# Performance work log

Measured on AMD Instinct MI355X. Metric: run time of the kernel, lower is better.

## Reference

```python
import jax, jax.numpy as jnp
import numpy as np

N = 50000       # nodes
E = 800000      # edges (before self-loops)
IN = 64         # in_channels
OUT = 64        # out_channels


def setup_inputs() -> dict:
    key = jax.random.key(0)
    ks = jax.random.split(key, 6)
    X = jax.random.normal(ks[0], (N, IN), jnp.float32)
    H = jax.random.normal(ks[1], (N, OUT), jnp.float32)
    edge_index = jax.random.randint(ks[2], (2, E), 0, N, dtype=jnp.int64)
    edge_weight = jax.random.uniform(ks[3], (E,), jnp.float32)
    fan_in = IN + OUT
    W1 = jax.random.normal(ks[4], (fan_in, 2 * OUT), jnp.float32) / np.sqrt(fan_in).astype(np.float32)
    b1 = jnp.ones((2 * OUT,), jnp.float32)   # TGCN sets graph_conv1.bias to ones
    W2 = jax.random.normal(ks[5], (fan_in, OUT), jnp.float32) / np.sqrt(fan_in).astype(np.float32)
    b2 = jnp.zeros((OUT,), jnp.float32)      # default GCNConv bias init
    return {"X": X, "H": H, "edge_index": edge_index, "edge_weight": edge_weight,
            "W1": W1, "b1": b1, "W2": W2, "b2": b2}


def _gcn_conv(x, W, b, src, dst, w, n):
    """PyG GCNConv: linear transform, add self-loops (fill=1, improved=False),
    symmetric deg^-1/2 normalization, scatter-add aggregation at dst, + bias."""
    x = x @ W                                   # [N, out]
    loop = jnp.arange(n, dtype=src.dtype)
    s = jnp.concatenate([src, loop])            # [E+N]
    d = jnp.concatenate([dst, loop])
    ww = jnp.concatenate([w, jnp.ones((n,), x.dtype)])
    deg = jax.ops.segment_sum(ww, d, num_segments=n)
    dinv = jnp.where(deg > 0, jax.lax.rsqrt(jnp.maximum(deg, 1e-12)), 0.0)
    norm = dinv[s] * ww * dinv[d]               # [E+N]
    msg = x[s] * norm[:, None]                  # gather + scale
    out = jax.ops.segment_sum(msg, d, num_segments=n)  # scatter-add at dst
    return out + b


def reference(X, H, edge_index, edge_weight, W1, b1, W2, b2):
    src, dst = edge_index[0], edge_index[1]
    n = X.shape[0]
    ru = jax.nn.sigmoid(_gcn_conv(jnp.concatenate([X, H], axis=1), W1, b1, src, dst, edge_weight, n))
    r, u = ru[:, :OUT], ru[:, OUT:]             # chunk into reset/update gates
    c = jnp.tanh(_gcn_conv(jnp.concatenate([X, H * r], axis=1), W2, b2, src, dst, edge_weight, n))
    return u * H + (1.0 - u) * c                # new hidden state [N, OUT]
```

## Files before the change

### kernel.cpp

```cpp
#include <hip/hip_runtime.h>
#include <hip/hip_bf16.h>
#include <hip/hip_fp16.h>

#define NN 50000
#define NE 800000
#define NBIN ((NN + 255) / 256)
#define PB ((NE + 1023) / 1024)
#define GB ((NN + 63) / 64)
#define MAXB 4864

__device__ __forceinline__ unsigned int f2bf(float x) {
    unsigned int u = __float_as_uint(x);
    return (u + 0x7FFFu + ((u >> 16) & 1u)) >> 16;
}
__device__ __forceinline__ float bf2f(unsigned int b) {
    return __uint_as_float(b << 16);
}

template <int OUTC, int NKC, int SRC, int OMODE>
__device__ __forceinline__ void gemm_core(
    const float* __restrict__ X, const float* __restrict__ Hm,
    const unsigned int* __restrict__ RUb, const float* __restrict__ W,
    const float* __restrict__ addF, const float* __restrict__ dinvp,
    uint2* __restrict__ outB, float* __restrict__ outF,
    int bid, float4* wS4, float4* inS4)
{
    constexpr int CG = OUTC / 4;
    constexpr int RSTEP = 256 / CG;
    constexpr int RPT = 64 / RSTEP;
    const int tid = threadIdx.x;
    const int cg = tid % CG;
    const int rsub = tid / CG;
    const int row0 = bid * 64;

    float4 acc[RPT];
    #pragma unroll
    for (int r = 0; r < RPT; ++r) acc[r] = {0.f, 0.f, 0.f, 0.f};

    for (int kc = 0; kc < NKC; ++kc) {
        const float4* Wg = reinterpret_cast<const float4*>(W + kc * 16 * OUTC);
        #pragma unroll
        for (int i = tid; i < 16 * CG; i += 256) wS4[i] = Wg[i];
        {
            int rr = tid >> 2, j = tid & 3;
            int row = row0 + rr;
            float4 v = {0.f, 0.f, 0.f, 0.f};
            if (row < NN) {
                int f4 = kc * 4 + j;
                if (SRC == 0) {
                    v = (f4 < 16) ? reinterpret_cast<const float4*>(X)[row * 16 + f4]
                                  : reinterpret_cast<const float4*>(Hm)[row * 16 + f4 - 16];
                } else if (SRC == 1) {
                    v = reinterpret_cast<const float4*>(X)[row * 16 + f4];
                } else {
                    v = reinterpret_cast<const float4*>(Hm)[row * 16 + f4];
                    unsigned int r0 = RUb[row * 64 + 2 * f4];
                    unsigned int r1 = RUb[row * 64 + 2 * f4 + 1];
                    v.x *= bf2f(r0 & 0xFFFFu); v.y *= bf2f(r0 >> 16);
                    v.z *= bf2f(r1 & 0xFFFFu); v.w *= bf2f(r1 >> 16);
                }
            }
            inS4[rr * 4 + j] = v;
        }
        __syncthreads();

        #pragma unroll
        for (int k8 = 0; k8 < 2; ++k8) {
            float4 wr[8];
            #pragma unroll
            for (int j = 0; j < 8; ++j) wr[j] = wS4[(k8 * 8 + j) * CG + cg];
            #pragma unroll
            for (int r = 0; r < RPT; ++r) {
                const int rr = rsub + r * RSTEP;
                float4 a0 = inS4[rr * 4 + k8 * 2];
                float4 a1 = inS4[rr * 4 + k8 * 2 + 1];
                acc[r].x += a0.x * wr[0].x; acc[r].y += a0.x * wr[0].y;
                acc[r].z += a0.x * wr[0].z; acc[r].w += a0.x * wr[0].w;
                acc[r].x += a0.y * wr[1].x; acc[r].y += a0.y * wr[1].y;
                acc[r].z += a0.y * wr[1].z; acc[r].w += a0.y * wr[1].w;
                acc[r].x += a0.z * wr[2].x; acc[r].y += a0.z * wr[2].y;
                acc[r].z += a0.z * wr[2].z; acc[r].w += a0.z * wr[2].w;
                acc[r].x += a0.w * wr[3].x; acc[r].y += a0.w * wr[3].y;
                acc[r].z += a0.w * wr[3].z; acc[r].w += a0.w * wr[3].w;
                acc[r].x += a1.x * wr[4].x; acc[r].y += a1.x * wr[4].y;
                acc[r].z += a1.x * wr[4].z; acc[r].w += a1.x * wr[4].w;
                acc[r].x += a1.y * wr[5].x; acc[r].y += a1.y * wr[5].y;
                acc[r].z += a1.y * wr[5].z; acc[r].w += a1.y * wr[5].w;
                acc[r].x += a1.z * wr[6].x; acc[r].y += a1.z * wr[6].y;
                acc[r].z += a1.z * wr[6].z; acc[r].w += a1.z * wr[6].w;
                acc[r].x += a1.w * wr[7].x; acc[r].y += a1.w * wr[7].y;
                acc[r].z += a1.w * wr[7].z; acc[r].w += a1.w * wr[7].w;
            }
        }
        __syncthreads();
    }

    #pragma unroll
    for (int r = 0; r < RPT; ++r) {
        int row = row0 + rsub + r * RSTEP;
        if (row < NN) {
            if (OMODE == 1) {
                reinterpret_cast<float4*>(outF)[(size_t)row * CG + cg] = acc[r];
            } else {
                float4 a = acc[r];
                if (OMODE == 2) {
                    float4 ad = reinterpret_cast<const float4*>(addF)[(size_t)row * CG + cg];
                    float dv = dinvp[row];
                    a.x = (a.x + ad.x) * dv; a.y = (a.y + ad.y) * dv;
                    a.z = (a.z + ad.z) * dv; a.w = (a.w + ad.w) * dv;
                }
                uint2 o;
                o.x = f2bf(a.x) | (f2bf(a.y) << 16);
                o.y = f2bf(a.z) | (f2bf(a.w) << 16);
                outB[(size_t)row * CG + cg] = o;
            }
        }
    }
}

__launch_bounds__(256)
__global__ void k_build(const float* __restrict__ X, const float* __restrict__ Hm,
                        const float* __restrict__ W1, const float* __restrict__ W2,
                        uint2* __restrict__ Z1b, float* __restrict__ Z2p,
                        const int* __restrict__ dst, int* __restrict__ HT) {
    __shared__ float4 wS4[512];
    __shared__ float4 inS4[256];
    const int bid = blockIdx.x;
    const int tid = threadIdx.x;
    if (bid < PB) {
        int* hist = reinterpret_cast<int*>(wS4);
        for (int i = tid; i < NBIN; i += 256) hist[i] = 0;
        __syncthreads();
        const int base = bid * 1024 + tid;
        #pragma unroll
        for (int k = 0; k < 4; ++k) {
            int e = base + k * 256;
            if (e < NE) atomicAdd(&hist[dst[e] >> 8], 1);
        }
        __syncthreads();
        for (int i = tid; i < NBIN; i += 256) HT[i * PB + bid] = hist[i];
        return;
    }
    if (bid < PB + GB) {
        gemm_core<128, 8, 0, 0>(X, Hm, nullptr, W1, nullptr, nullptr, Z1b, nullptr,
                                bid - PB, wS4, inS4);
        return;
    }
    gemm_core<64, 4, 1, 1>(X, Hm, nullptr, W2, nullptr, nullptr, nullptr, Z2p,
                           bid - PB - GB, wS4, inS4);
}

__launch_bounds__(256)
__global__ void k_scanA1(const int* __restrict__ HT, int* __restrict__ within,
                         int* __restrict__ binTot) {
    __shared__ int lds[PB];
    __shared__ int sc[256];
    __shared__ int carryS;
    const int b = blockIdx.x, tid = threadIdx.x;
    if (tid == 0) carryS = 0;
    for (int i = tid; i < PB; i += 256) lds[i] = HT[b * PB + i];
    __syncthreads();
    for (int c0 = 0; c0 < PB; c0 += 256) {
        int i = c0 + tid;
        int v = (i < PB) ? lds[i] : 0;
        sc[tid] = v;
        __syncthreads();
        #pragma unroll
        for (int off = 1; off < 256; off <<= 1) {
            int t = (tid >= off) ? sc[tid - off] : 0;
            __syncthreads();
            sc[tid] += t;
            __syncthreads();
        }
        int carry = carryS;
        if (i < PB) lds[i] = carry + sc[tid] - v;
        __syncthreads();
        if (tid == 255) carryS = carry + sc[255];
        __syncthreads();
    }
    for (int i = tid; i < PB; i += 256) within[b * PB + i] = lds[i];
    if (tid == 0) binTot[b] = carryS;
}

__launch_bounds__(256)
__global__ void k_scanA2(const int* __restrict__ binTot, int* __restrict__ binStart) {
    __shared__ int sc[256];
    const int tid = threadIdx.x;
    int v = (tid < NBIN) ? binTot[tid] : 0;
    sc[tid] = v;
    __syncthreads();
    #pragma unroll
    for (int off = 1; off < 256; off <<= 1) {
        int t = (tid >= off) ? sc[tid - off] : 0;
        __syncthreads();
        sc[tid] += t;
        __syncthreads();
    }
    if (tid < NBIN) binStart[tid] = sc[tid] - v;
    if (tid == 0) binStart[NBIN] = NE;
}

__launch_bounds__(256)
__global__ void k_scatterA(const int* __restrict__ src, const int* __restrict__ dst,
                           const float* __restrict__ w, const int* __restrict__ binStart,
                           const int* __restrict__ within, uint2* __restrict__ rec) {
    __shared__ int cur[NBIN];
    const int blk = blockIdx.x, tid = threadIdx.x;
    for (int b = tid; b < NBIN; b += 256) cur[b] = binStart[b] + within[b * PB + blk];
    __syncthreads();
    const int base = blk * 1024 + tid;
    #pragma unroll
    for (int k = 0; k < 4; ++k) {
        int e = base + k * 256;
        if (e < NE) {
            int d = dst[e];
            int pos = atomicAdd(&cur[d >> 8], 1);
            unsigned int hn = __half_as_ushort(__float2half(w[e]));
            uint2 r;
            r.x = (unsigned int)src[e] | (hn << 16);
            r.y = (unsigned int)d;
            rec[pos] = r;
        }
    }
}

__launch_bounds__(256)
__global__ void k_phase2(const uint2* __restrict__ rec, const int* __restrict__ binStart,
                         unsigned int* __restrict__ snP, int* __restrict__ start,
                         float* __restrict__ dinv, uint2* __restrict__ Z1b) {
    __shared__ unsigned int rSn[MAXB];
    __shared__ unsigned char rLo[MAXB];
    __shared__ unsigned int outSn[MAXB];
    __shared__ int cnt[256];
    __shared__ int sc[256];
    __shared__ int lstart[256];
    __shared__ int cur[256];
    __shared__ float dls[256];
    const int b = blockIdx.x, tid = threadIdx.x;
    const int e0 = binStart[b];
    int nE = binStart[b + 1] - e0;
    if (nE > MAXB) nE = MAXB;

    cnt[tid] = 0;
    __syncthreads();
    for (int i = tid; i < nE; i += 256) {
        uint2 r = rec[e0 + i];
        rSn[i] = r.x;
        int lo = r.y & 255;
        rLo[i] = (unsigned char)lo;
        atomicAdd(&cnt[lo], 1);
    }
    __syncthreads();
    sc[tid] = cnt[tid];
    __syncthreads();
    #pragma unroll
    for (int off = 1; off < 256; off <<= 1) {
        int t = (tid >= off) ? sc[tid - off] : 0;
        __syncthreads();
        sc[tid] += t;
        __syncthreads();
    }
    lstart[tid] = sc[tid] - cnt[tid];
    cur[tid] = sc[tid] - cnt[tid];
    __syncthreads();
    const int node = b * 256 + tid;
    if (node <= NN) start[node] = e0 + lstart[tid];
    for (int i = tid; i < nE; i += 256) {
        int p = atomicAdd(&cur[rLo[i]], 1);
        outSn[p] = rSn[i];
    }
    __syncthreads();
    for (int i = tid; i < nE; i += 256) snP[e0 + i] = outSn[i];
    {
        int s0 = lstart[tid], c = cnt[tid];
        float sum = 0.f;
        for (int i = s0; i < s0 + c; ++i)
            sum += __half2float(__ushort_as_half((unsigned short)(outSn[i] >> 16)));
        float dv = rsqrtf(1.0f + sum);
        dls[tid] = dv;
        if (node < NN) dinv[node] = dv;
    }
    __syncthreads();
    const int nLoc = (NN - b * 256 < 256) ? (NN - b * 256) : 256;
    for (int i = tid; i < nLoc * 32; i += 256) {
        int l = i >> 5, j = i & 31;
        size_t g = (size_t)(b * 256 + l) * 32 + j;
        uint2 z = Z1b[g];
        float dv = dls[l];
        float z0 = bf2f(z.x & 0xFFFFu) * dv, z1 = bf2f(z.x >> 16) * dv;
        float z2 = bf2f(z.y & 0xFFFFu) * dv, z3 = bf2f(z.y >> 16) * dv;
        uint2 o;
        o.x = f2bf(z0) | (f2bf(z1) << 16);
        o.y = f2bf(z2) | (f2bf(z3) << 16);
        Z1b[g] = o;
    }
}

__launch_bounds__(256)
__global__ void k_gemm2b(const float* __restrict__ X, const float* __restrict__ Hm,
                         const unsigned int* __restrict__ RUb, const float* __restrict__ W2,
                         const float* __restrict__ Z2p, const float* __restrict__ dinv,
                         uint2* __restrict__ Z2b) {
    __shared__ float4 wS4[256];
    __shared__ float4 inS4[256];
    gemm_core<64, 4, 2, 2>(X, Hm, RUb, W2 + 64 * 64, Z2p, dinv, Z2b, nullptr,
                           blockIdx.x, wS4, inS4);
}

template <int OUTC, int MODE>
__launch_bounds__(256)
__global__ void k_gather(const int* __restrict__ start, const unsigned int* __restrict__ snP,
                         const uint2* __restrict__ Zb, const float* __restrict__ dinv,
                         const float* __restrict__ bias, const uint2* __restrict__ RUb2,
                         uint2* __restrict__ outB, const float* __restrict__ Hm,
                         float* __restrict__ out) {
    constexpr int GRP = OUTC / 4;
    constexpr int NPB = 256 / GRP;
    const int node = blockIdx.x * NPB + threadIdx.x / GRP;
    const int l = threadIdx.x % GRP;
    if (node >= NN) return;

    const int e0 = start[node], e1 = start[node + 1];

    uint2 zs = Zb[(size_t)node * GRP + l];
    float4 acc;
    acc.x = bf2f(zs.x & 0xFFFFu);
    acc.y = bf2f(zs.x >> 16);
    acc.z = bf2f(zs.y & 0xFFFFu);
    acc.w = bf2f(zs.y >> 16);

    #define EFMA(Z, NM) \
        acc.x += bf2f((Z).x & 0xFFFFu) * (NM); \
        acc.y += bf2f((Z).x >> 16) * (NM);     \
        acc.z += bf2f((Z).y & 0xFFFFu) * (NM); \
        acc.w += bf2f((Z).y >> 16) * (NM);

    int e = e0;
    for (; e + 8 <= e1; e += 8) {
        unsigned sn0 = snP[e],     sn1 = snP[e + 1], sn2 = snP[e + 2], sn3 = snP[e + 3];
        unsigned sn4 = snP[e + 4], sn5 = snP[e + 5], sn6 = snP[e + 6], sn7 = snP[e + 7];
        uint2 z0 = Zb[(size_t)(sn0 & 0xFFFFu) * GRP + l];
        uint2 z1 = Zb[(size_t)(sn1 & 0xFFFFu) * GRP + l];
        uint2 z2 = Zb[(size_t)(sn2 & 0xFFFFu) * GRP + l];
        uint2 z3 = Zb[(size_t)(sn3 & 0xFFFFu) * GRP + l];
        uint2 z4 = Zb[(size_t)(sn4 & 0xFFFFu) * GRP + l];
        uint2 z5 = Zb[(size_t)(sn5 & 0xFFFFu) * GRP + l];
        uint2 z6 = Zb[(size_t)(sn6 & 0xFFFFu) * GRP + l];
        uint2 z7 = Zb[(size_t)(sn7 & 0xFFFFu) * GRP + l];
        float n0 = __half2float(__ushort_as_half((unsigned short)(sn0 >> 16)));
        float n1 = __half2float(__ushort_as_half((unsigned short)(sn1 >> 16)));
        float n2 = __half2float(__ushort_as_half((unsigned short)(sn2 >> 16)));
        float n3 = __half2float(__ushort_as_half((unsigned short)(sn3 >> 16)));
        float n4 = __half2float(__ushort_as_half((unsigned short)(sn4 >> 16)));
        float n5 = __half2float(__ushort_as_half((unsigned short)(sn5 >> 16)));
        float n6 = __half2float(__ushort_as_half((unsigned short)(sn6 >> 16)));
        float n7 = __half2float(__ushort_as_half((unsigned short)(sn7 >> 16)));
        EFMA(z0, n0) EFMA(z1, n1) EFMA(z2, n2) EFMA(z3, n3)
        EFMA(z4, n4) EFMA(z5, n5) EFMA(z6, n6) EFMA(z7, n7)
    }
    if (e + 4 <= e1) {
        unsigned sn0 = snP[e], sn1 = snP[e + 1], sn2 = snP[e + 2], sn3 = snP[e + 3];
        uint2 z0 = Zb[(size_t)(sn0 & 0xFFFFu) * GRP + l];
        uint2 z1 = Zb[(size_t)(sn1 & 0xFFFFu) * GRP + l];
        uint2 z2 = Zb[(size_t)(sn2 & 0xFFFFu) * GRP + l];
        uint2 z3 = Zb[(size_t)(sn3 & 0xFFFFu) * GRP + l];
        float n0 = __half2float(__ushort_as_half((unsigned short)(sn0 >> 16)));
        float n1 = __half2float(__ushort_as_half((unsigned short)(sn1 >> 16)));
        float n2 = __half2float(__ushort_as_half((unsigned short)(sn2 >> 16)));
        float n3 = __half2float(__ushort_as_half((unsigned short)(sn3 >> 16)));
        EFMA(z0, n0) EFMA(z1, n1) EFMA(z2, n2) EFMA(z3, n3)
        e += 4;
    }
    for (; e < e1; ++e) {
        unsigned sn = snP[e];
        float nm = __half2float(__ushort_as_half((unsigned short)(sn >> 16)));
        uint2 z = Zb[(size_t)(sn & 0xFFFFu) * GRP + l];
        EFMA(z, nm)
    }
    #undef EFMA

    const float dv = dinv[node];
    const int c = l * 4;
    float4 bb = *reinterpret_cast<const float4*>(bias + c);
    acc.x = acc.x * dv + bb.x; acc.y = acc.y * dv + bb.y;
    acc.z = acc.z * dv + bb.z; acc.w = acc.w * dv + bb.w;

    if (MODE == 0) {
        float4 o;
        o.x = 1.f / (1.f + expf(-acc.x));
        o.y = 1.f / (1.f + expf(-acc.y));
        o.z = 1.f / (1.f + expf(-acc.z));
        o.w = 1.f / (1.f + expf(-acc.w));
        uint2 pk;
        pk.x = f2bf(o.x) | (f2bf(o.y) << 16);
        pk.y = f2bf(o.z) | (f2bf(o.w) << 16);
        outB[(size_t)node * 32 + l] = pk;
    } else {
        uint2 uu = RUb2[(size_t)node * 32 + 16 + l];
        float u0 = bf2f(uu.x & 0xFFFFu), u1 = bf2f(uu.x >> 16);
        float u2 = bf2f(uu.y & 0xFFFFu), u3 = bf2f(uu.y >> 16);
        float4 h4 = *reinterpret_cast<const float4*>(Hm + (size_t)node * 64 + c);
        float4 o;
        o.x = u0 * h4.x + (1.f - u0) * tanhf(acc.x);
        o.y = u1 * h4.y + (1.f - u1) * tanhf(acc.y);
        o.z = u2 * h4.z + (1.f - u2) * tanhf(acc.z);
        o.w = u3 * h4.w + (1.f - u3) * tanhf(acc.w);
        *reinterpret_cast<float4*>(out + (size_t)node * 64 + c) = o;
    }
}

extern "C" void kernel_launch(void* const* d_in, const int* in_sizes, int n_in,
                              void* d_out, int out_size, void* d_ws, size_t ws_size,
                              hipStream_t stream) {
    const float* X  = (const float*)d_in[0];
    const float* Hm = (const float*)d_in[1];
    const int*   ei = (const int*)d_in[2];
    const float* w  = (const float*)d_in[3];
    const float* W1 = (const float*)d_in[4];
    const float* b1 = (const float*)d_in[5];
    const float* W2 = (const float*)d_in[6];
    const float* b2 = (const float*)d_in[7];
    float* out = (float*)d_out;

    const int* src = ei;
    const int* dst = ei + NE;

    char* p = (char*)d_ws;
    uint2* rec   = (uint2*)p;  p += sizeof(uint2) * NE;
    uint2* Z1b   = (uint2*)p;  p += sizeof(uint2) * NN * 32;
    uint2* Z2b   = (uint2*)p;  p += sizeof(uint2) * NN * 16;
    uint2* RUb2  = (uint2*)p;  p += sizeof(uint2) * NN * 32;
    float* Z2p   = (float*)p;  p += sizeof(float) * NN * 64;
    float* dinv  = (float*)p;  p += sizeof(float) * NN;
    int*   start = (int*)p;    p += sizeof(int) * (NN + 1);
    int*   binTot   = (int*)p; p += sizeof(int) * NBIN;
    int*   binStart = (int*)p; p += sizeof(int) * (NBIN + 1);
    int*   HT       = (int*)p; p += sizeof(int) * NBIN * PB;
    int*   within   = (int*)p; p += sizeof(int) * NBIN * PB;
    unsigned int* snP = (unsigned int*)p; p += sizeof(unsigned int) * NE;

    k_build<<<PB + 2 * GB, 256, 0, stream>>>(X, Hm, W1, W2, Z1b, Z2p, dst, HT);

    k_scanA1<<<NBIN, 256, 0, stream>>>(HT, within, binTot);
    k_scanA2<<<1, 256, 0, stream>>>(binTot, binStart);
    k_scatterA<<<PB, 256, 0, stream>>>(src, dst, w, binStart, within, rec);
    k_phase2<<<NBIN, 256, 0, stream>>>(rec, binStart, snP, start, dinv, Z1b);

    k_gather<128, 0><<<(NN * 32 + 255) / 256, 256, 0, stream>>>(
        start, snP, Z1b, dinv, b1, nullptr, RUb2, nullptr, nullptr);

    k_gemm2b<<<GB, 256, 0, stream>>>(X, Hm, (const unsigned int*)RUb2, W2, Z2p, dinv, Z2b);
    k_gather<64, 1><<<(NN * 16 + 255) / 256, 256, 0, stream>>>(
        start, snP, Z2b, dinv, b2, RUb2, nullptr, Hm, out);
}
```

Measured before the change: 140.6 us.

## Replace FP32 FMA GEMMs with bf16 MFMA using prepacked weight fragments

Adds a small kernel that converts W1 and W2 to bf16 and lays them out in MFMA fragment order. The three dense GEMMs now stage bf16 input tiles in LDS and run 16x16x32 bf16 MFMA instructions instead of scalar FP32 FMAs. This removes the scalar-FMA compute cost of the GEMM stages but adds an extra kernel launch. Inputs are also rounded to bf16 before multiplying, which lowers precision, and the epilogue now writes scalar 16-bit stores instead of packed vector stores.

```diff
diff --git a/kernel.cpp b/kernel.cpp
--- a/kernel.cpp
+++ b/kernel.cpp
@@ -9,6 +9,9 @@
 #define GB ((NN + 63) / 64)
 #define MAXB 4864
 
+typedef __attribute__((ext_vector_type(8))) short bf16x8;
+typedef __attribute__((ext_vector_type(4))) float f32x4;
+
 __device__ __forceinline__ unsigned int f2bf(float x) {
     unsigned int u = __float_as_uint(x);
     return (u + 0x7FFFu + ((u >> 16) & 1u)) >> 16;
@@ -17,118 +20,134 @@
     return __uint_as_float(b << 16);
 }
 
-template <int OUTC, int NKC, int SRC, int OMODE>
-__device__ __forceinline__ void gemm_core(
+__global__ void k_wprep(const float* __restrict__ W1, const float* __restrict__ W2,
+                        unsigned short* __restrict__ Wf1,
+                        unsigned short* __restrict__ Wf2t,
+                        unsigned short* __restrict__ Wf2b) {
+    int i = blockIdx.x * 256 + threadIdx.x;
+    if (i < 16384) {
+        int j = i & 7, l = (i >> 3) & 63, n = (i >> 9) & 7, kc = i >> 12;
+        int k = kc * 32 + ((l >> 4) << 3) + j;
+        int col = (n << 4) + (l & 15);
+        Wf1[i] = (unsigned short)f2bf(W1[k * 128 + col]);
+    }
+    if (i < 4096) {
+        int j = i & 7, l = (i >> 3) & 63, n = (i >> 9) & 3, kc = i >> 11;
+        int k = kc * 32 + ((l >> 4) << 3) + j;
+        int col = (n << 4) + (l & 15);
+        Wf2t[i] = (unsigned short)f2bf(W2[k * 64 + col]);
+        Wf2b[i] = (unsigned short)f2bf(W2[(k + 64) * 64 + col]);
+    }
+}
+
+template <int OUTC, int KC, int SRC, int OMODE>
+__device__ __forceinline__ void mgemm_core(
     const float* __restrict__ X, const float* __restrict__ Hm,
-    const unsigned int* __restrict__ RUb, const float* __restrict__ W,
-    const float* __restrict__ addF, const float* __restrict__ dinvp,
-    uint2* __restrict__ outB, float* __restrict__ outF,
-    int bid, float4* wS4, float4* inS4)
+    const unsigned int* __restrict__ RUb, const unsigned short* __restrict__ Wf,
+    const float* __restrict__ Z2p, const float* __restrict__ dinv,
+    unsigned short* __restrict__ outH, float* __restrict__ outF,
+    int bid, unsigned short* aS, unsigned short* wS)
 {
-    constexpr int CG = OUTC / 4;
-    constexpr int RSTEP = 256 / CG;
-    constexpr int RPT = 64 / RSTEP;
+    constexpr int NT = OUTC / 16;
     const int tid = threadIdx.x;
-    const int cg = tid % CG;
-    const int rsub = tid / CG;
     const int row0 = bid * 64;
 
-    float4 acc[RPT];
-    #pragma unroll
-    for (int r = 0; r < RPT; ++r) acc[r] = {0.f, 0.f, 0.f, 0.f};
-
-    for (int kc = 0; kc < NKC; ++kc) {
-        const float4* Wg = reinterpret_cast<const float4*>(W + kc * 16 * OUTC);
-        #pragma unroll
-        for (int i = tid; i < 16 * CG; i += 256) wS4[i] = Wg[i];
-        {
-            int rr = tid >> 2, j = tid & 3;
-            int row = row0 + rr;
-            float4 v = {0.f, 0.f, 0.f, 0.f};
-            if (row < NN) {
-                int f4 = kc * 4 + j;
-                if (SRC == 0) {
-                    v = (f4 < 16) ? reinterpret_cast<const float4*>(X)[row * 16 + f4]
-                                  : reinterpret_cast<const float4*>(Hm)[row * 16 + f4 - 16];
-                } else if (SRC == 1) {
-                    v = reinterpret_cast<const float4*>(X)[row * 16 + f4];
-                } else {
-                    v = reinterpret_cast<const float4*>(Hm)[row * 16 + f4];
-                    unsigned int r0 = RUb[row * 64 + 2 * f4];
-                    unsigned int r1 = RUb[row * 64 + 2 * f4 + 1];
-                    v.x *= bf2f(r0 & 0xFFFFu); v.y *= bf2f(r0 >> 16);
-                    v.z *= bf2f(r1 & 0xFFFFu); v.w *= bf2f(r1 >> 16);
-                }
+    constexpr int WH = KC * NT * 64 * 8;
+    {
+        const uint4* Wg4 = reinterpret_cast<const uint4*>(Wf);
+        uint4* wS4 = reinterpret_cast<uint4*>(wS);
+        #pragma unroll
+        for (int i = tid; i < WH / 8; i += 256) wS4[i] = Wg4[i];
+    }
+    #pragma unroll
+    for (int i = tid; i < 64 * KC * 8; i += 256) {
+        int row = i / (KC * 8), f4 = i % (KC * 8);
+        int g = row0 + row;
+        float4 v = {0.f, 0.f, 0.f, 0.f};
+        if (g < NN) {
+            if (SRC == 0) {
+                v = (f4 < 16) ? reinterpret_cast<const float4*>(X)[g * 16 + f4]
+                              : reinterpret_cast<const float4*>(Hm)[g * 16 + f4 - 16];
+            } else if (SRC == 1) {
+                v = reinterpret_cast<const float4*>(X)[g * 16 + f4];
+            } else {
+                v = reinterpret_cast<const float4*>(Hm)[g * 16 + f4];
+                unsigned int r0 = RUb[g * 64 + 2 * f4];
+                unsigned int r1 = RUb[g * 64 + 2 * f4 + 1];
+                v.x *= bf2f(r0 & 0xFFFFu); v.y *= bf2f(r0 >> 16);
+                v.z *= bf2f(r1 & 0xFFFFu); v.w *= bf2f(r1 >> 16);
             }
-            inS4[rr * 4 + j] = v;
-        }
-        __syncthreads();
-
-        #pragma unroll
-        for (int k8 = 0; k8 < 2; ++k8) {
-            float4 wr[8];
-            #pragma unroll
-            for (int j = 0; j < 8; ++j) wr[j] = wS4[(k8 * 8 + j) * CG + cg];
-            #pragma unroll
-            for (int r = 0; r < RPT; ++r) {
-                const int rr = rsub + r * RSTEP;
-                float4 a0 = inS4[rr * 4 + k8 * 2];
-                float4 a1 = inS4[rr * 4 + k8 * 2 + 1];
-                acc[r].x += a0.x * wr[0].x; acc[r].y += a0.x * wr[0].y;
-                acc[r].z += a0.x * wr[0].z; acc[r].w += a0.x * wr[0].w;
-                acc[r].x += a0.y * wr[1].x; acc[r].y += a0.y * wr[1].y;
-                acc[r].z += a0.y * wr[1].z; acc[r].w += a0.y * wr[1].w;
-                acc[r].x += a0.z * wr[2].x; acc[r].y += a0.z * wr[2].y;
-                acc[r].z += a0.z * wr[2].z; acc[r].w += a0.z * wr[2].w;
-                acc[r].x += a0.w * wr[3].x; acc[r].y += a0.w * wr[3].y;
-                acc[r].z += a0.w * wr[3].z; acc[r].w += a0.w * wr[3].w;
-                acc[r].x += a1.x * wr[4].x; acc[r].y += a1.x * wr[4].y;
-                acc[r].z += a1.x * wr[4].z; acc[r].w += a1.x * wr[4].w;
-                acc[r].x += a1.y * wr[5].x; acc[r].y += a1.y * wr[5].y;
-                acc[r].z += a1.y * wr[5].z; acc[r].w += a1.y * wr[5].w;
-                acc[r].x += a1.z * wr[6].x; acc[r].y += a1.z * wr[6].y;
-                acc[r].z += a1.z * wr[6].z; acc[r].w += a1.z * wr[6].w;
-                acc[r].x += a1.w * wr[7].x; acc[r].y += a1.w * wr[7].y;
-                acc[r].z += a1.w * wr[7].z; acc[r].w += a1.w * wr[7].w;
+        }
+        int k = f4 * 4;
+        int kc = k >> 5, ko = k & 31;
+        int l = (row & 15) | ((ko >> 3) << 4);
+        int j0 = ko & 7;
+        int m = row >> 4;
+        uint2 pk;
+        pk.x = f2bf(v.x) | (f2bf(v.y) << 16);
+        pk.y = f2bf(v.z) | (f2bf(v.w) << 16);
+        *reinterpret_cast<uint2*>(aS + (((m * KC + kc) * 64 + l) * 8 + j0)) = pk;
+    }
+    __syncthreads();
+
+    const int wid = tid >> 6, l = tid & 63;
+    f32x4 acc[NT];
+    #pragma unroll
+    for (int n = 0; n < NT; ++n) acc[n] = {0.f, 0.f, 0.f, 0.f};
+
+    const bf16x8* aF = reinterpret_cast<const bf16x8*>(aS);
+    const bf16x8* wF = reinterpret_cast<const bf16x8*>(wS);
+    #pragma unroll
+    for (int kc = 0; kc < KC; ++kc) {
+        bf16x8 a = aF[(wid * KC + kc) * 64 + l];
+        #pragma unroll
+        for (int n = 0; n < NT; ++n) {
+            bf16x8 b = wF[(kc * NT + n) * 64 + l];
+            acc[n] = __builtin_amdgcn_mfma_f32_16x16x32_bf16(a, b, acc[n], 0, 0, 0);
+        }
+    }
+
+    const int rbase = row0 + wid * 16 + ((l >> 4) << 2);
+    const int cl = l & 15;
+    float dv[4];
+    if (OMODE == 2) {
+        #pragma unroll
+        for (int i = 0; i < 4; ++i) {
+            int row = rbase + i;
+            dv[i] = (row < NN) ? dinv[row] : 0.f;
+        }
+    }
+    #pragma unroll
+    for (int n = 0; n < NT; ++n) {
+        #pragma unroll
+        for (int i = 0; i < 4; ++i) {
+            int row = rbase + i;
+            if (row >= NN) continue;
+            int col = n * 16 + cl;
+            if (OMODE == 0) {
+                outH[(size_t)row * OUTC + col] = (unsigned short)f2bf(acc[n][i]);
+            } else if (OMODE == 1) {
+                outF[(size_t)row * OUTC + col] = acc[n][i];
+            } else {
+                float a2 = (acc[n][i] + Z2p[(size_t)row * 64 + col]) * dv[i];
+                outH[(size_t)row * 64 + col] = (unsigned short)f2bf(a2);
             }
         }
-        __syncthreads();
-    }
-
-    #pragma unroll
-    for (int r = 0; r < RPT; ++r) {
-        int row = row0 + rsub + r * RSTEP;
-        if (row < NN) {
-            if (OMODE == 1) {
-                reinterpret_cast<float4*>(outF)[(size_t)row * CG + cg] = acc[r];
-            } else {
-                float4 a = acc[r];
-                if (OMODE == 2) {
-                    float4 ad = reinterpret_cast<const float4*>(addF)[(size_t)row * CG + cg];
-                    float dv = dinvp[row];
-                    a.x = (a.x + ad.x) * dv; a.y = (a.y + ad.y) * dv;
-                    a.z = (a.z + ad.z) * dv; a.w = (a.w + ad.w) * dv;
-                }
-                uint2 o;
-                o.x = f2bf(a.x) | (f2bf(a.y) << 16);
-                o.y = f2bf(a.z) | (f2bf(a.w) << 16);
-                outB[(size_t)row * CG + cg] = o;
-            }
-        }
     }
 }
 
 __launch_bounds__(256)
 __global__ void k_build(const float* __restrict__ X, const float* __restrict__ Hm,
-                        const float* __restrict__ W1, const float* __restrict__ W2,
-                        uint2* __restrict__ Z1b, float* __restrict__ Z2p,
+                        const unsigned short* __restrict__ Wf1,
+                        const unsigned short* __restrict__ Wf2t,
+                        unsigned short* __restrict__ Z1b, float* __restrict__ Z2p,
                         const int* __restrict__ dst, int* __restrict__ HT) {
-    __shared__ float4 wS4[512];
-    __shared__ float4 inS4[256];
+    __shared__ unsigned short aS[8192];
+    __shared__ unsigned short wS[16384];
     const int bid = blockIdx.x;
     const int tid = threadIdx.x;
     if (bid < PB) {
-        int* hist = reinterpret_cast<int*>(wS4);
+        int* hist = reinterpret_cast<int*>(aS);
         for (int i = tid; i < NBIN; i += 256) hist[i] = 0;
         __syncthreads();
         const int base = bid * 1024 + tid;
@@ -142,12 +161,24 @@
         return;
     }
     if (bid < PB + GB) {
-        gemm_core<128, 8, 0, 0>(X, Hm, nullptr, W1, nullptr, nullptr, Z1b, nullptr,
-                                bid - PB, wS4, inS4);
+        mgemm_core<128, 4, 0, 0>(X, Hm, nullptr, Wf1, nullptr, nullptr,
+                                 Z1b, nullptr, bid - PB, aS, wS);
         return;
     }
-    gemm_core<64, 4, 1, 1>(X, Hm, nullptr, W2, nullptr, nullptr, nullptr, Z2p,
-                           bid - PB - GB, wS4, inS4);
+    mgemm_core<64, 2, 1, 1>(X, Hm, nullptr, Wf2t, nullptr, nullptr,
+                            nullptr, Z2p, bid - PB - GB, aS, wS);
+}
+
+__launch_bounds__(256)
+__global__ void k_gemm2b(const float* __restrict__ X, const float* __restrict__ Hm,
+                         const unsigned int* __restrict__ RUb,
+                         const unsigned short* __restrict__ Wf2b,
+                         const float* __restrict__ Z2p, const float* __restrict__ dinv,
+                         unsigned short* __restrict__ Z2b) {
+    __shared__ unsigned short aS[4096];
+    __shared__ unsigned short wS[4096];
+    mgemm_core<64, 2, 2, 2>(X, Hm, RUb, Wf2b, Z2p, dinv, Z2b, nullptr,
+                            blockIdx.x, aS, wS);
 }
 
 __launch_bounds__(256)
@@ -294,17 +325,6 @@
         o.y = f2bf(z2) | (f2bf(z3) << 16);
         Z1b[g] = o;
     }
-}
-
-__launch_bounds__(256)
-__global__ void k_gemm2b(const float* __restrict__ X, const float* __restrict__ Hm,
-                         const unsigned int* __restrict__ RUb, const float* __restrict__ W2,
-                         const float* __restrict__ Z2p, const float* __restrict__ dinv,
-                         uint2* __restrict__ Z2b) {
-    __shared__ float4 wS4[256];
-    __shared__ float4 inS4[256];
-    gemm_core<64, 4, 2, 2>(X, Hm, RUb, W2 + 64 * 64, Z2p, dinv, Z2b, nullptr,
-                           blockIdx.x, wS4, inS4);
 }
 
 template <int OUTC, int MODE>
@@ -438,8 +458,14 @@
     int*   HT       = (int*)p; p += sizeof(int) * NBIN * PB;
     int*   within   = (int*)p; p += sizeof(int) * NBIN * PB;
     unsigned int* snP = (unsigned int*)p; p += sizeof(unsigned int) * NE;
-
-    k_build<<<PB + 2 * GB, 256, 0, stream>>>(X, Hm, W1, W2, Z1b, Z2p, dst, HT);
+    unsigned short* Wf1  = (unsigned short*)p; p += sizeof(unsigned short) * 16384;
+    unsigned short* Wf2t = (unsigned short*)p; p += sizeof(unsigned short) * 4096;
+    unsigned short* Wf2b = (unsigned short*)p; p += sizeof(unsigned short) * 4096;
+
+    k_wprep<<<64, 256, 0, stream>>>(W1, W2, Wf1, Wf2t, Wf2b);
+
+    k_build<<<PB + 2 * GB, 256, 0, stream>>>(X, Hm, Wf1, Wf2t,
+                                             (unsigned short*)Z1b, Z2p, dst, HT);
 
     k_scanA1<<<NBIN, 256, 0, stream>>>(HT, within, binTot);
     k_scanA2<<<1, 256, 0, stream>>>(binTot, binStart);
@@ -449,7 +475,8 @@
     k_gather<128, 0><<<(NN * 32 + 255) / 256, 256, 0, stream>>>(
         start, snP, Z1b, dinv, b1, nullptr, RUb2, nullptr, nullptr);
 
-    k_gemm2b<<<GB, 256, 0, stream>>>(X, Hm, (const unsigned int*)RUb2, W2, Z2p, dinv, Z2b);
+    k_gemm2b<<<GB, 256, 0, stream>>>(X, Hm, (const unsigned int*)RUb2, Wf2b,
+                                     Z2p, dinv, (unsigned short*)Z2b);
     k_gather<64, 1><<<(NN * 16 + 255) / 256, 256, 0, stream>>>(
         start, snP, Z2b, dinv, b2, RUb2, nullptr, Hm, out);
 }
```

Result: faster. 127.0 us (-9.6%).
